# Performance work log

Measured on AMD Instinct MI355X. Metric: run time of the kernel, lower is better.

The kernel has to match this reference:

```python
import jax, jax.numpy as jnp
import numpy as np

B, L, S, H, E = 4, 1024, 1024, 8, 64


def setup_inputs() -> dict:
    key = jax.random.key(0)
    ks = jax.random.split(key, 8)
    return {
        "query": jax.random.normal(ks[0], (B, L, H, E), dtype=jnp.float32),
        "key": jax.random.normal(ks[1], (B, S, H, E), dtype=jnp.float32),
        "value": jax.random.normal(ks[2], (B, S, H, E), dtype=jnp.float32),
        "phi": jax.random.normal(ks[3], (H, L, S), dtype=jnp.float32),
        "log_gain": jnp.asarray(np.log(10.0), dtype=jnp.float32),
        "log_tau": jnp.asarray(np.log(2.0), dtype=jnp.float32),
        "log_tau_comm": jnp.asarray(np.log(0.2), dtype=jnp.float32),
        "hard_mask": jax.random.uniform(ks[4], (L, S), dtype=jnp.float32),
        "u": jax.random.uniform(ks[5], (H, L, S), dtype=jnp.float32),
        "mask_miss_k": jnp.ones((B, S), dtype=jnp.float32),
        "mask_miss_q": jnp.ones((B, L), dtype=jnp.float32),
        "pos": jnp.zeros((B, L), dtype=jnp.float32),
        "causal_mask": 0,
    }


def reference(query, key, value, phi, log_gain, log_tau, log_tau_comm,
              hard_mask, u, mask_miss_k, mask_miss_q, pos, causal_mask):
    # mask_miss_k/q, pos, causal_mask are unused by LieAttention.forward (torch parity)
    E_dim = query.shape[-1]
    scale = 1.0 / float(np.sqrt(E_dim))
    # raw scores (B, H, L, S)
    scores = jnp.einsum('blhe,bshe->bhls', query, key)
    # antisymmetric communication term
    comm = scores - jnp.swapaxes(scores, -1, -2)
    gain = jnp.clip(jnp.exp(log_gain), 1e-3, 1000.0)      # max_gain = 1000
    tau_comm = jnp.clip(jnp.exp(log_tau_comm), 1e-3, 10.0)
    comm_amp = jnp.tanh((gain / tau_comm) * comm)
    att = scale * jax.nn.gelu(comm_amp, approximate=False)  # torch F.gelu = exact erf
    # Gumbel-sigmoid relaxed DAG mask, broadcast over batch: M (1, H, L, S)
    tau = jnp.clip(jnp.exp(log_tau), 0.1, 5.0)             # tau_min/tau_max
    m_relaxed = jax.nn.sigmoid((jnp.log(u + 1e-8) - jnp.log(1.0 - u + 1e-8) + phi) / tau)
    att = att * m_relaxed[None]
    # hard mask (L, S) -> (1, 1, L, S)
    att = att * hard_mask[None, None]
    # attention entropy per query position: (B, H, L)
    eps = 1e-8
    entropy = jnp.nan_to_num(-jnp.sum(att * jnp.log(jnp.maximum(att, eps)), axis=-1))
    A = jnp.nan_to_num(att)  # dropout=0.0 -> identity
    V = jnp.einsum('bhls,bshd->blhd', A, value)
    return V, A, entropy
```

## Files before the change

### kernel.cpp

```cpp
#include <hip/hip_runtime.h>
#include <math.h>

#define Bn 4
#define Ln 1024
#define Sn 1024
#define Hn 8
#define En 64

typedef __attribute__((ext_vector_type(4))) float f32x4;
typedef __attribute__((ext_vector_type(8))) _Float16 h16x8;
typedef __attribute__((ext_vector_type(4))) _Float16 h16x4;

__device__ __forceinline__ float frcp(float x) { return __builtin_amdgcn_rcpf(x); }

__device__ __forceinline__ void gl_lds16(const void* g, void* l) {
    __builtin_amdgcn_global_load_lds(
        (const __attribute__((address_space(1))) unsigned int*)g,
        (__attribute__((address_space(3))) unsigned int*)l, 16, 0, 0);
}

__global__ __launch_bounds__(256) void prep(
    const float* __restrict__ Q, const float* __restrict__ K,
    const float* __restrict__ V,
    _Float16* __restrict__ Qh, _Float16* __restrict__ Ql,
    _Float16* __restrict__ Kh, _Float16* __restrict__ Kl,
    _Float16* __restrict__ Vt) {
    __shared__ float vlds[64][69];
    const int st = blockIdx.x;
    const int bh = blockIdx.y;
    const int b = bh >> 3, h = bh & 7;
    const int tid = threadIdx.x;
    const int s0 = st * 64;

#pragma unroll
    for (int i = 0; i < 4; ++i) {
        int idx = tid + 256 * i;
        int r = idx >> 4;
        int c4 = (idx & 15) << 2;
        size_t gin = (((size_t)b * Ln + s0 + r) * Hn + h) * En + c4;
        f32x4 qv = *(const f32x4*)(Q + gin);
        f32x4 kv = *(const f32x4*)(K + gin);
        f32x4 vv = *(const f32x4*)(V + gin);
        vlds[r][c4 + 0] = vv.x; vlds[r][c4 + 1] = vv.y;
        vlds[r][c4 + 2] = vv.z; vlds[r][c4 + 3] = vv.w;
        h16x4 qh4, ql4, kh4, kl4;
#pragma unroll
        for (int j = 0; j < 4; ++j) {
            float x = qv[j];
            _Float16 hx = (_Float16)x;
            qh4[j] = hx; ql4[j] = (_Float16)(x - (float)hx);
            float y = kv[j];
            _Float16 hy = (_Float16)y;
            kh4[j] = hy; kl4[j] = (_Float16)(y - (float)hy);
        }
        size_t ob = ((size_t)bh * 1024 + s0 + r) * 64 + ((((c4 >> 3) ^ (r & 7)) << 3) + (c4 & 7));
        *(h16x4*)(Qh + ob) = qh4; *(h16x4*)(Ql + ob) = ql4;
        *(h16x4*)(Kh + ob) = kh4; *(h16x4*)(Kl + ob) = kl4;
    }
    __syncthreads();
#pragma unroll
    for (int i = 0; i < 4; ++i) {
        int idx = tid + 256 * i;
        int d = idx >> 4;
        int sg = (idx & 15) << 2;
        h16x4 v4;
#pragma unroll
        for (int j = 0; j < 4; ++j) v4[j] = (_Float16)vlds[sg + j][d];
        size_t ob = (((size_t)bh * 16 + st) * 64 + d) * 64 + ((((sg >> 3) ^ (d & 7)) << 3) + (sg & 7));
        *(h16x4*)(Vt + ob) = v4;
    }
}

__global__ __launch_bounds__(256, 3) void fused_lie(
    const _Float16* __restrict__ Qh, const _Float16* __restrict__ Ql,
    const _Float16* __restrict__ Kh, const _Float16* __restrict__ Kl,
    const _Float16* __restrict__ Vt,
    const float* __restrict__ phi, const float* __restrict__ u,
    const float* __restrict__ hard,
    const float* __restrict__ p_lg, const float* __restrict__ p_lt,
    const float* __restrict__ p_ltc,
    float* __restrict__ Aout, float* __restrict__ Vout,
    float* __restrict__ entOut) {
    __shared__ __align__(16) _Float16 kbh[4096];
    __shared__ __align__(16) _Float16 kbl[4096];
    __shared__ __align__(16) _Float16 qbh[4096];
    __shared__ __align__(16) _Float16 qbl[4096];
    __shared__ __align__(16) _Float16 vbt[4096];
    __shared__ __align__(16) _Float16 plds[4][16 * 72];

    const int bx = blockIdx.x;
    const int lt = bx >> 1, sh = bx & 1;
    const int h = blockIdx.y, b = blockIdx.z;
    const int bh = b * Hn + h;
    const int tid = threadIdx.x;
    const int w = tid >> 6;
    const int lane = tid & 63;
    const int q = lane >> 4;
    const int n = lane & 15;
    const int swz = n & 7;
    const int l0 = lt * 64;

    const float gain = fminf(fmaxf(expf(p_lg[0]), 1e-3f), 1000.0f);
    const float tauc = fminf(fmaxf(expf(p_ltc[0]), 1e-3f), 10.0f);
    const float c2 = 2.0f * gain / tauc;
    const float tau = fminf(fmaxf(expf(p_lt[0]), 0.1f), 5.0f);
    const float itau = 1.0f / tau;

    h16x8 QAh[2], QAl[2], KAh[2], KAl[2];
    {
        const size_t ab = ((size_t)bh * 1024 + l0 + w * 16 + n) * 64;
#pragma unroll
        for (int kh = 0; kh < 2; ++kh) {
            size_t off = ab + (((q + kh * 4) ^ swz) << 3);
            QAh[kh] = *(const h16x8*)(Qh + off);
            QAl[kh] = *(const h16x8*)(Ql + off);
            KAh[kh] = *(const h16x8*)(Kh + off);
            KAl[kh] = *(const h16x8*)(Kl + off);
        }
    }

    f32x4 accV[4];
#pragma unroll
    for (int i = 0; i < 4; ++i) accV[i] = (f32x4){0.f, 0.f, 0.f, 0.f};
    float entp[4] = {0.f, 0.f, 0.f, 0.f};

    const int lbase = l0 + w * 16 + q * 4;

    for (int stc = 0; stc < 8; ++stc) {
        const int st = sh * 8 + stc;
        const int s0 = st * 64;
        if (stc) __syncthreads();

        {
            const size_t sb = ((size_t)bh * 1024 + s0) * 64;
            const size_t vb = (((size_t)bh * 16 + st) * 64) * 64;
#pragma unroll
            for (int i = 0; i < 2; ++i) {
                int hoff = w * 1024 + i * 512 + lane * 8;
                gl_lds16(Kh + sb + hoff, kbh + hoff);
                gl_lds16(Kl + sb + hoff, kbl + hoff);
                gl_lds16(Qh + sb + hoff, qbh + hoff);
                gl_lds16(Ql + sb + hoff, qbl + hoff);
                gl_lds16(Vt + vb + hoff, vbt + hoff);
            }
        }
        __syncthreads();

        f32x4 a1[4], a2[4];
#pragma unroll
        for (int i = 0; i < 4; ++i) {
            a1[i] = (f32x4){0.f, 0.f, 0.f, 0.f};
            a2[i] = (f32x4){0.f, 0.f, 0.f, 0.f};
        }
#pragma unroll
        for (int kh = 0; kh < 2; ++kh) {
#pragma unroll
            for (int sub = 0; sub < 4; ++sub) {
                const int off = (sub * 16 + n) * 64 + (((q + kh * 4) ^ swz) << 3);
                h16x8 KBh = *(const h16x8*)&kbh[off];
                h16x8 KBl = *(const h16x8*)&kbl[off];
                h16x8 QBh = *(const h16x8*)&qbh[off];
                h16x8 QBl = *(const h16x8*)&qbl[off];
                f32x4 x1 = a1[sub], x2 = a2[sub];
                x1 = __builtin_amdgcn_mfma_f32_16x16x32_f16(QAh[kh], KBh, x1, 0, 0, 0);
                x1 = __builtin_amdgcn_mfma_f32_16x16x32_f16(QAh[kh], KBl, x1, 0, 0, 0);
                x1 = __builtin_amdgcn_mfma_f32_16x16x32_f16(QAl[kh], KBh, x1, 0, 0, 0);
                x2 = __builtin_amdgcn_mfma_f32_16x16x32_f16(KAh[kh], QBh, x2, 0, 0, 0);
                x2 = __builtin_amdgcn_mfma_f32_16x16x32_f16(KAh[kh], QBl, x2, 0, 0, 0);
                x2 = __builtin_amdgcn_mfma_f32_16x16x32_f16(KAl[kh], QBh, x2, 0, 0, 0);
                a1[sub] = x1; a2[sub] = x2;
            }
        }

#pragma unroll
        for (int sub = 0; sub < 4; ++sub) {
            const int s = s0 + sub * 16 + n;
#pragma unroll
            for (int r = 0; r < 4; ++r) {
                const int l = lbase + r;
                const size_t pidx = ((size_t)h * Ln + l) * (size_t)Sn + s;
                float ph = phi[pidx];
                float uu = u[pidx];
                float hm = hard[(size_t)l * Sn + s];
                float cm = a1[sub][r] - a2[sub][r];
                float x = 1.0f - 2.0f * frcp(__expf(c2 * cm) + 1.0f);
                float t = x * fmaf(0.044715f * x, x, 1.0f);
                float g = x * frcp(1.0f + __expf(-1.59576912161f * t));
                float z = (__logf((uu + 1e-8f) * frcp(1.0f - uu + 1e-8f)) + ph) * itau;
                float m = frcp(1.0f + __expf(-z));
                float att = 0.125f * g * m * hm;
                Aout[(((size_t)b * Hn + h) * Ln + l) * (size_t)Sn + s] = att;
                entp[r] += att * __logf(fmaxf(att, 1e-8f));
                plds[w][(q * 4 + r) * 72 + sub * 16 + n] = (_Float16)att;
            }
        }

        {
            const _Float16* pw = &plds[w][0];
#pragma unroll
            for (int kh = 0; kh < 2; ++kh) {
                h16x8 Pf = *(const h16x8*)&pw[n * 72 + q * 8 + kh * 32];
#pragma unroll
                for (int sub = 0; sub < 4; ++sub) {
                    h16x8 Vf = *(const h16x8*)&vbt[(sub * 16 + n) * 64 + (((q + kh * 4) ^ swz) << 3)];
                    accV[sub] = __builtin_amdgcn_mfma_f32_16x16x32_f16(Pf, Vf, accV[sub], 0, 0, 0);
                }
            }
        }
    }

#pragma unroll
    for (int sub = 0; sub < 4; ++sub) {
#pragma unroll
        for (int r = 0; r < 4; ++r) {
            const int l = l0 + w * 16 + q * 4 + r;
            atomicAdd(Vout + (((size_t)b * Ln + l) * Hn + h) * En + sub * 16 + n, accV[sub][r]);
        }
    }
#pragma unroll
    for (int r = 0; r < 4; ++r) {
        float v = entp[r];
        v += __shfl_xor(v, 1);
        v += __shfl_xor(v, 2);
        v += __shfl_xor(v, 4);
        v += __shfl_xor(v, 8);
        if (n == 0) {
            atomicAdd(entOut + ((size_t)b * Hn + h) * Ln + lbase + r, -v);
        }
    }
}

extern "C" void kernel_launch(void* const* d_in, const int* in_sizes, int n_in,
                              void* d_out, int out_size, void* d_ws, size_t ws_size,
                              hipStream_t stream) {
    (void)in_sizes; (void)n_in; (void)ws_size; (void)out_size;

    const float* Q    = (const float*)d_in[0];
    const float* K    = (const float*)d_in[1];
    const float* Vv   = (const float*)d_in[2];
    const float* phi  = (const float*)d_in[3];
    const float* lg   = (const float*)d_in[4];
    const float* ltau = (const float*)d_in[5];
    const float* ltc  = (const float*)d_in[6];
    const float* hard = (const float*)d_in[7];
    const float* u    = (const float*)d_in[8];

    float* out  = (float*)d_out;
    float* Vout = out;
    float* Aout = out + (size_t)Bn * Ln * Hn * En;
    float* ent  = Aout + (size_t)Bn * Hn * Ln * Sn;

    const size_t NE = (size_t)32 * 1024 * 64;
    _Float16* Qh = (_Float16*)d_ws;
    _Float16* Ql = Qh + NE;
    _Float16* Kh = Ql + NE;
    _Float16* Kl = Kh + NE;
    _Float16* Vt = Kl + NE;

    hipMemsetAsync(Vout, 0, (size_t)Bn * Ln * Hn * En * sizeof(float), stream);
    hipMemsetAsync(ent, 0, (size_t)Bn * Hn * Ln * sizeof(float), stream);
    prep<<<dim3(16, 32), 256, 0, stream>>>(Q, K, Vv, Qh, Ql, Kh, Kl, Vt);
    fused_lie<<<dim3(32, Hn, Bn), 256, 0, stream>>>(Qh, Ql, Kh, Kl, Vt, phi, u, hard,
                                                    lg, ltau, ltc, Aout, Vout, ent);
}
```

Before: 337.6 us.

## Precompute batch-invariant fp16 DAG mask and read Q/K/V tiles directly from global

Adds a prep kernel that computes the Gumbel-sigmoid mask times hard mask times scale once per head into an fp16 buffer, so the fused kernel no longer recomputes logs and sigmoids per batch. The fused kernel drops LDS staging of K/Q/V tiles and reads a new tiled layout straight from global memory, removing barriers and raising occupancy. It also switches to raw exp2/log2 instructions with folded constants. In exchange it adds an extra pass and fp16 rounding of the mask, and relies on cache for the repeated tile reads.

```diff
diff --git a/kernel.cpp b/kernel.cpp
--- a/kernel.cpp
+++ b/kernel.cpp
@@ -12,11 +12,11 @@
 typedef __attribute__((ext_vector_type(4))) _Float16 h16x4;
 
 __device__ __forceinline__ float frcp(float x) { return __builtin_amdgcn_rcpf(x); }
-
-__device__ __forceinline__ void gl_lds16(const void* g, void* l) {
-    __builtin_amdgcn_global_load_lds(
-        (const __attribute__((address_space(1))) unsigned int*)g,
-        (__attribute__((address_space(3))) unsigned int*)l, 16, 0, 0);
+__device__ __forceinline__ float fexp2(float x) {
+    float r; asm("v_exp_f32 %0, %1" : "=v"(r) : "v"(x)); return r;
+}
+__device__ __forceinline__ float flog2(float x) {
+    float r; asm("v_log_f32 %0, %1" : "=v"(r) : "v"(x)); return r;
 }
 
 __global__ __launch_bounds__(256) void prep(
@@ -53,7 +53,7 @@
             _Float16 hy = (_Float16)y;
             kh4[j] = hy; kl4[j] = (_Float16)(y - (float)hy);
         }
-        size_t ob = ((size_t)bh * 1024 + s0 + r) * 64 + ((((c4 >> 3) ^ (r & 7)) << 3) + (c4 & 7));
+        size_t ob = ((((size_t)bh * 16 + st) * 8 + (c4 >> 3)) * 64 + r) * 8 + (c4 & 7);
         *(h16x4*)(Qh + ob) = qh4; *(h16x4*)(Ql + ob) = ql4;
         *(h16x4*)(Kh + ob) = kh4; *(h16x4*)(Kl + ob) = kl4;
     }
@@ -66,26 +66,48 @@
         h16x4 v4;
 #pragma unroll
         for (int j = 0; j < 4; ++j) v4[j] = (_Float16)vlds[sg + j][d];
-        size_t ob = (((size_t)bh * 16 + st) * 64 + d) * 64 + ((((sg >> 3) ^ (d & 7)) << 3) + (sg & 7));
+        size_t ob = ((((size_t)bh * 16 + st) * 8 + (sg >> 3)) * 64 + d) * 8 + (sg & 7);
         *(h16x4*)(Vt + ob) = v4;
     }
 }
 
-__global__ __launch_bounds__(256, 3) void fused_lie(
+__global__ __launch_bounds__(256) void prep2(
+    const float* __restrict__ phi, const float* __restrict__ u,
+    const float* __restrict__ hard, const float* __restrict__ p_lt,
+    _Float16* __restrict__ mh) {
+    const float tau = fminf(fmaxf(expf(p_lt[0]), 0.1f), 5.0f);
+    const float itau = 1.0f / tau;
+    const size_t base = ((size_t)blockIdx.x * 256 + threadIdx.x) * 8;
+    const size_t ls = base & (size_t)(Ln * Sn - 1);
+    f32x4 ph0 = *(const f32x4*)(phi + base);
+    f32x4 ph1 = *(const f32x4*)(phi + base + 4);
+    f32x4 uu0 = *(const f32x4*)(u + base);
+    f32x4 uu1 = *(const f32x4*)(u + base + 4);
+    f32x4 hm0 = *(const f32x4*)(hard + ls);
+    f32x4 hm1 = *(const f32x4*)(hard + ls + 4);
+    h16x8 o;
+#pragma unroll
+    for (int j = 0; j < 4; ++j) {
+        float z = (__logf((uu0[j] + 1e-8f) * frcp(1.0f - uu0[j] + 1e-8f)) + ph0[j]) * itau;
+        float m = frcp(1.0f + __expf(-z));
+        o[j] = (_Float16)(0.125f * m * hm0[j]);
+    }
+#pragma unroll
+    for (int j = 0; j < 4; ++j) {
+        float z = (__logf((uu1[j] + 1e-8f) * frcp(1.0f - uu1[j] + 1e-8f)) + ph1[j]) * itau;
+        float m = frcp(1.0f + __expf(-z));
+        o[4 + j] = (_Float16)(0.125f * m * hm1[j]);
+    }
+    *(h16x8*)(mh + base) = o;
+}
+
+__global__ __launch_bounds__(256, 4) void fused_lie(
     const _Float16* __restrict__ Qh, const _Float16* __restrict__ Ql,
     const _Float16* __restrict__ Kh, const _Float16* __restrict__ Kl,
-    const _Float16* __restrict__ Vt,
-    const float* __restrict__ phi, const float* __restrict__ u,
-    const float* __restrict__ hard,
-    const float* __restrict__ p_lg, const float* __restrict__ p_lt,
-    const float* __restrict__ p_ltc,
+    const _Float16* __restrict__ Vt, const _Float16* __restrict__ mh,
+    const float* __restrict__ p_lg, const float* __restrict__ p_ltc,
     float* __restrict__ Aout, float* __restrict__ Vout,
     float* __restrict__ entOut) {
-    __shared__ __align__(16) _Float16 kbh[4096];
-    __shared__ __align__(16) _Float16 kbl[4096];
-    __shared__ __align__(16) _Float16 qbh[4096];
-    __shared__ __align__(16) _Float16 qbl[4096];
-    __shared__ __align__(16) _Float16 vbt[4096];
     __shared__ __align__(16) _Float16 plds[4][16 * 72];
 
     const int bx = blockIdx.x;
@@ -97,21 +119,18 @@
     const int lane = tid & 63;
     const int q = lane >> 4;
     const int n = lane & 15;
-    const int swz = n & 7;
     const int l0 = lt * 64;
 
     const float gain = fminf(fmaxf(expf(p_lg[0]), 1e-3f), 1000.0f);
     const float tauc = fminf(fmaxf(expf(p_ltc[0]), 1e-3f), 10.0f);
-    const float c2 = 2.0f * gain / tauc;
-    const float tau = fminf(fmaxf(expf(p_lt[0]), 0.1f), 5.0f);
-    const float itau = 1.0f / tau;
+    const float c2l = 2.0f * gain / tauc * 1.44269504f;
 
     h16x8 QAh[2], QAl[2], KAh[2], KAl[2];
     {
-        const size_t ab = ((size_t)bh * 1024 + l0 + w * 16 + n) * 64;
+        const size_t ab = (((size_t)bh * 16 + lt) * 8) * 512 + (size_t)(w * 16 + n) * 8;
 #pragma unroll
         for (int kh = 0; kh < 2; ++kh) {
-            size_t off = ab + (((q + kh * 4) ^ swz) << 3);
+            size_t off = ab + (size_t)(q + 4 * kh) * 512;
             QAh[kh] = *(const h16x8*)(Qh + off);
             QAl[kh] = *(const h16x8*)(Ql + off);
             KAh[kh] = *(const h16x8*)(Kh + off);
@@ -125,26 +144,13 @@
     float entp[4] = {0.f, 0.f, 0.f, 0.f};
 
     const int lbase = l0 + w * 16 + q * 4;
+    float* __restrict__ arow = Aout + (((size_t)b * Hn + h) * Ln + lbase) * (size_t)Sn;
+    const _Float16* __restrict__ ment = mh + ((size_t)h * Ln + lbase) * (size_t)Sn;
 
     for (int stc = 0; stc < 8; ++stc) {
         const int st = sh * 8 + stc;
         const int s0 = st * 64;
-        if (stc) __syncthreads();
-
-        {
-            const size_t sb = ((size_t)bh * 1024 + s0) * 64;
-            const size_t vb = (((size_t)bh * 16 + st) * 64) * 64;
-#pragma unroll
-            for (int i = 0; i < 2; ++i) {
-                int hoff = w * 1024 + i * 512 + lane * 8;
-                gl_lds16(Kh + sb + hoff, kbh + hoff);
-                gl_lds16(Kl + sb + hoff, kbl + hoff);
-                gl_lds16(Qh + sb + hoff, qbh + hoff);
-                gl_lds16(Ql + sb + hoff, qbl + hoff);
-                gl_lds16(Vt + vb + hoff, vbt + hoff);
-            }
-        }
-        __syncthreads();
+        const size_t tb = (((size_t)bh * 16 + st) * 8) * 512;
 
         f32x4 a1[4], a2[4];
 #pragma unroll
@@ -154,13 +160,14 @@
         }
 #pragma unroll
         for (int kh = 0; kh < 2; ++kh) {
+            const size_t kqb = tb + (size_t)(q + 4 * kh) * 512;
 #pragma unroll
             for (int sub = 0; sub < 4; ++sub) {
-                const int off = (sub * 16 + n) * 64 + (((q + kh * 4) ^ swz) << 3);
-                h16x8 KBh = *(const h16x8*)&kbh[off];
-                h16x8 KBl = *(const h16x8*)&kbl[off];
-                h16x8 QBh = *(const h16x8*)&qbh[off];
-                h16x8 QBl = *(const h16x8*)&qbl[off];
+                const size_t off = kqb + (size_t)(sub * 16 + n) * 8;
+                h16x8 KBh = *(const h16x8*)(Kh + off);
+                h16x8 KBl = *(const h16x8*)(Kl + off);
+                h16x8 QBh = *(const h16x8*)(Qh + off);
+                h16x8 QBl = *(const h16x8*)(Ql + off);
                 f32x4 x1 = a1[sub], x2 = a2[sub];
                 x1 = __builtin_amdgcn_mfma_f32_16x16x32_f16(QAh[kh], KBh, x1, 0, 0, 0);
                 x1 = __builtin_amdgcn_mfma_f32_16x16x32_f16(QAh[kh], KBl, x1, 0, 0, 0);
@@ -177,36 +184,33 @@
             const int s = s0 + sub * 16 + n;
 #pragma unroll
             for (int r = 0; r < 4; ++r) {
-                const int l = lbase + r;
-                const size_t pidx = ((size_t)h * Ln + l) * (size_t)Sn + s;
-                float ph = phi[pidx];
-                float uu = u[pidx];
-                float hm = hard[(size_t)l * Sn + s];
+                float mhv = (float)ment[(size_t)r * Sn + s];
                 float cm = a1[sub][r] - a2[sub][r];
-                float x = 1.0f - 2.0f * frcp(__expf(c2 * cm) + 1.0f);
+                float x = 1.0f - 2.0f * frcp(fexp2(c2l * cm) + 1.0f);
                 float t = x * fmaf(0.044715f * x, x, 1.0f);
-                float g = x * frcp(1.0f + __expf(-1.59576912161f * t));
-                float z = (__logf((uu + 1e-8f) * frcp(1.0f - uu + 1e-8f)) + ph) * itau;
-                float m = frcp(1.0f + __expf(-z));
-                float att = 0.125f * g * m * hm;
-                Aout[(((size_t)b * Hn + h) * Ln + l) * (size_t)Sn + s] = att;
-                entp[r] += att * __logf(fmaxf(att, 1e-8f));
+                float g = x * frcp(1.0f + fexp2(-2.30221271f * t));
+                float att = g * mhv;
+                arow[(size_t)r * Sn + s] = att;
+                entp[r] += att * flog2(fmaxf(att, 1e-8f));
                 plds[w][(q * 4 + r) * 72 + sub * 16 + n] = (_Float16)att;
             }
         }
+        asm volatile("" ::: "memory");
 
         {
             const _Float16* pw = &plds[w][0];
 #pragma unroll
             for (int kh = 0; kh < 2; ++kh) {
+                const size_t kqb = tb + (size_t)(q + 4 * kh) * 512;
                 h16x8 Pf = *(const h16x8*)&pw[n * 72 + q * 8 + kh * 32];
 #pragma unroll
                 for (int sub = 0; sub < 4; ++sub) {
-                    h16x8 Vf = *(const h16x8*)&vbt[(sub * 16 + n) * 64 + (((q + kh * 4) ^ swz) << 3)];
+                    h16x8 Vf = *(const h16x8*)(Vt + kqb + (size_t)(sub * 16 + n) * 8);
                     accV[sub] = __builtin_amdgcn_mfma_f32_16x16x32_f16(Pf, Vf, accV[sub], 0, 0, 0);
                 }
             }
         }
+        asm volatile("" ::: "memory");
     }
 
 #pragma unroll
@@ -225,7 +229,7 @@
         v += __shfl_xor(v, 4);
         v += __shfl_xor(v, 8);
         if (n == 0) {
-            atomicAdd(entOut + ((size_t)b * Hn + h) * Ln + lbase + r, -v);
+            atomicAdd(entOut + ((size_t)b * Hn + h) * Ln + lbase + r, -v * 0.69314718f);
         }
     }
 }
@@ -256,10 +260,12 @@
     _Float16* Kh = Ql + NE;
     _Float16* Kl = Kh + NE;
     _Float16* Vt = Kl + NE;
+    _Float16* mh = Vt + NE;
 
     hipMemsetAsync(Vout, 0, (size_t)Bn * Ln * Hn * En * sizeof(float), stream);
     hipMemsetAsync(ent, 0, (size_t)Bn * Hn * Ln * sizeof(float), stream);
     prep<<<dim3(16, 32), 256, 0, stream>>>(Q, K, Vv, Qh, Ql, Kh, Kl, Vt);
-    fused_lie<<<dim3(32, Hn, Bn), 256, 0, stream>>>(Qh, Ql, Kh, Kl, Vt, phi, u, hard,
-                                                    lg, ltau, ltc, Aout, Vout, ent);
-}
+    prep2<<<dim3(4096), 256, 0, stream>>>(phi, u, hard, ltau, mh);
+    fused_lie<<<dim3(32, Hn, Bn), 256, 0, stream>>>(Qh, Ql, Kh, Kl, Vt, mh,
+                                                    lg, ltc, Aout, Vout, ent);
+}
```

Result: slower. 363.6 us (+7.7%).
